# Performance work log

Hardware: AMD Instinct MI355X
Metric: run time of the kernel (lower is better)

Reference implementation:

```python
import jax, jax.numpy as jnp
import numpy as np
from itertools import product

# problem dims
B, D = 2, 80            # batch, grid side -> 2*80^3 = 1.024M voxel slots
N = 200000
CIN, COUT = 32, 64
KV = 27                 # 3x3x3 kernel volume


def _build_rulebook():
    """Submanifold conv rulebook: in_idx[k, j] = input row whose coord equals
    coord_j + offset_k, or N (zero pad row) if that voxel is empty/out of grid."""
    rng = np.random.default_rng(0)
    total = B * D ** 3
    flat = rng.choice(total, size=N, replace=False)
    b, rem = flat // D ** 3, flat % D ** 3
    x, y, z = rem // (D * D), (rem // D) % D, rem % D
    lookup = np.full(total, N, dtype=np.int64)  # empty -> pad index N
    lookup[flat] = np.arange(N)
    rows = []
    for dx, dy, dz in product((-1, 0, 1), repeat=3):  # kernel offsets, dilation=1
        nx, ny, nz = x + dx, y + dy, z + dz
        valid = (0 <= nx) & (nx < D) & (0 <= ny) & (ny < D) & (0 <= nz) & (nz < D)
        nflat = ((b * D + nx) * D + ny) * D + nz
        rows.append(np.where(valid, lookup[np.clip(nflat, 0, total - 1)], N))
    return np.stack(rows).astype(np.int32)  # [KV, N]


def setup_inputs() -> dict:
    key = jax.random.key(0)
    k1, k2, k3 = jax.random.split(key, 3)
    stdv = 1.0 / float(np.sqrt(CIN * KV))  # matches reset_parameters
    feats = jax.random.normal(k1, (N, CIN), dtype=jnp.float32)
    weight = jax.random.uniform(k2, (KV, CIN, COUT), jnp.float32, -stdv, stdv)
    bias = jax.random.uniform(k3, (COUT,), jnp.float32, -stdv, stdv)
    in_idx = jnp.asarray(_build_rulebook())
    return {"feats": feats, "weight": weight, "bias": bias, "in_idx": in_idx}


def reference(feats, weight, bias, in_idx):
    # pad row N = zeros so missing neighbors contribute nothing
    feats_pad = jnp.concatenate(
        [feats, jnp.zeros((1, feats.shape[1]), feats.dtype)], axis=0)  # [N+1, Cin]

    def body(acc, kw):  # scan over the 27 kernel offsets: gather -> matmul -> accumulate
        idx_k, w_k = kw                       # [N] int32, [Cin, Cout]
        return acc + feats_pad[idx_k] @ w_k, None

    out0 = jnp.zeros((feats.shape[0], weight.shape[2]), feats.dtype)  # [N, Cout]
    out, _ = jax.lax.scan(body, out0, (in_idx, weight))
    return out + bias
```

## Files before the change

### kernel.cpp

```cpp
#include <hip/hip_runtime.h>
#include <cstddef>
#include <cstdint>

#define NROWS  200000
#define CIN    32
#define COUT   64
#define KV     27
#define NWAVES (NROWS / 64)

typedef __attribute__((ext_vector_type(8))) short  short8;
typedef __attribute__((ext_vector_type(4))) float  f32x4;

__device__ __forceinline__ unsigned short f2bf(float x) {
  unsigned u = __builtin_bit_cast(unsigned, x);
  u += 0x7FFFu + ((u >> 16) & 1u);
  return (unsigned short)(u >> 16);
}

__global__ void prep_weight_kernel(const float* __restrict__ w,
                                   short8* __restrict__ wsB) {
  int tid = blockIdx.x * blockDim.x + threadIdx.x;
  if (tid >= KV * 4 * 64) return;
  int lane = tid & 63;
  int t    = (tid >> 6) & 3;
  int k    = tid >> 8;
  int col  = t * 16 + (lane & 15);
  int kin0 = (lane >> 4) * 8;
  short8 v;
#pragma unroll
  for (int f = 0; f < 8; ++f)
    v[f] = (short)f2bf(w[((size_t)k * CIN + kin0 + f) * COUT + col]);
  wsB[tid] = v;
}

__global__ void prep_feats_kernel(const float* __restrict__ feats,
                                  short8* __restrict__ fb) {
  int i = blockIdx.x * blockDim.x + threadIdx.x;
  const int total8 = (NROWS + 1) * CIN / 8;
  if (i >= total8) return;
  short8 v = {0, 0, 0, 0, 0, 0, 0, 0};
  if (i < NROWS * CIN / 8) {
    const f32x4* p = (const f32x4*)feats + (size_t)i * 2;
    f32x4 a = p[0], b = p[1];
#pragma unroll
    for (int f = 0; f < 4; ++f) {
      v[f]     = (short)f2bf(a[f]);
      v[4 + f] = (short)f2bf(b[f]);
    }
  }
  fb[i] = v;
}

__global__ __launch_bounds__(256, 3)
void spconv_mfma_kernel(const unsigned short* __restrict__ featsbf,
                        const short8* __restrict__ wsB,
                        const float* __restrict__ bias,
                        const int* __restrict__ in_idx,
                        float* __restrict__ out) {
  __shared__ int sIdx[4][KV][64];

  const int tid  = threadIdx.x;
  const int lane = tid & 63;
  const int w    = tid >> 6;
  const int wid  = (int)blockIdx.x * 4 + w;
  if (wid >= NWAVES) return;
  const int row0 = wid << 6;

  {
    int tmp[KV];
#pragma unroll
    for (int k = 0; k < KV; ++k)
      tmp[k] = in_idx[(size_t)k * NROWS + row0 + lane];
#pragma unroll
    for (int k = 0; k < KV; ++k)
      sIdx[w][k][lane] = tmp[k];
  }

  const int c16  = lane & 15;
  const int kg   = lane >> 4;
  const int koff = kg * 8;

  f32x4 acc[4][4];
#pragma unroll
  for (int t = 0; t < 4; ++t) {
    float bv = bias[t * 16 + c16];
    f32x4 bvv = {bv, bv, bv, bv};
#pragma unroll
    for (int m = 0; m < 4; ++m) acc[m][t] = bvv;
  }

  const short8* bp = wsB + lane;

#pragma unroll 3
  for (int k = 0; k < KV; ++k) {
    int idx[4];
#pragma unroll
    for (int m = 0; m < 4; ++m) idx[m] = sIdx[w][k][m * 16 + c16];

    short8 bfr[4];
#pragma unroll
    for (int t = 0; t < 4; ++t) bfr[t] = bp[(k * 4 + t) * 64];

    short8 afr[4];
#pragma unroll
    for (int m = 0; m < 4; ++m)
      afr[m] = *(const short8*)(featsbf + (size_t)idx[m] * CIN + koff);

#pragma unroll
    for (int m = 0; m < 4; ++m) {
      acc[m][0] = __builtin_amdgcn_mfma_f32_16x16x32_bf16(afr[m], bfr[0], acc[m][0], 0, 0, 0);
      acc[m][1] = __builtin_amdgcn_mfma_f32_16x16x32_bf16(afr[m], bfr[1], acc[m][1], 0, 0, 0);
      acc[m][2] = __builtin_amdgcn_mfma_f32_16x16x32_bf16(afr[m], bfr[2], acc[m][2], 0, 0, 0);
      acc[m][3] = __builtin_amdgcn_mfma_f32_16x16x32_bf16(afr[m], bfr[3], acc[m][3], 0, 0, 0);
    }
  }

#pragma unroll
  for (int m = 0; m < 4; ++m)
#pragma unroll
    for (int t = 0; t < 4; ++t)
#pragma unroll
      for (int r = 0; r < 4; ++r)
        out[(size_t)(row0 + m * 16 + kg * 4 + r) * COUT + t * 16 + c16] = acc[m][t][r];
}

__global__ void spconv_naive_kernel(const float* __restrict__ feats,
                                    const float* __restrict__ w,
                                    const float* __restrict__ bias,
                                    const int* __restrict__ in_idx,
                                    float* __restrict__ out) {
  int gid = blockIdx.x * blockDim.x + threadIdx.x;
  if (gid >= NROWS * COUT) return;
  int row = gid / COUT, co = gid % COUT;
  float acc = bias[co];
  for (int k = 0; k < KV; ++k) {
    int idx = in_idx[(size_t)k * NROWS + row];
    if (idx < NROWS) {
      const float* fr = feats + (size_t)idx * CIN;
      const float* wk = w + (size_t)k * CIN * COUT + co;
#pragma unroll
      for (int c = 0; c < CIN; ++c) acc += fr[c] * wk[(size_t)c * COUT];
    }
  }
  out[gid] = acc;
}

extern "C" void kernel_launch(void* const* d_in, const int* in_sizes, int n_in,
                              void* d_out, int out_size, void* d_ws, size_t ws_size,
                              hipStream_t stream) {
  const float* feats  = (const float*)d_in[0];
  const float* weight = (const float*)d_in[1];
  const float* bias   = (const float*)d_in[2];
  const int*   in_idx = (const int*)d_in[3];
  float*       out    = (float*)d_out;

  const size_t wsB_bytes = (size_t)KV * 4 * 64 * 16;
  const size_t fb_bytes  = (size_t)(NROWS + 1) * CIN * 2;
  short8*         wsB     = (short8*)d_ws;
  unsigned short* featsbf = (unsigned short*)((char*)d_ws + wsB_bytes);

  if (ws_size >= wsB_bytes + fb_bytes) {
    prep_weight_kernel<<<27, 256, 0, stream>>>(weight, wsB);
    prep_feats_kernel<<<((NROWS + 1) * CIN / 8 + 255) / 256, 256, 0, stream>>>(
        feats, (short8*)featsbf);
    const int blocks = (NWAVES + 3) / 4;
    spconv_mfma_kernel<<<blocks, 256, 0, stream>>>(
        featsbf, wsB, bias, in_idx, out);
  } else {
    spconv_naive_kernel<<<(NROWS * COUT + 255) / 256, 256, 0, stream>>>(
        feats, weight, bias, in_idx, out);
  }
}
```

Baseline: 59.07 us.

## Stage all conv weights in LDS and split index staging into halves

Each 768-thread block (12 waves) first copies the full pre-swizzled bf16 weight tensor (27 offsets x 4 column tiles) from global memory into shared memory, so B fragments come from LDS instead of global/L2. To leave LDS room for this, the per-wave rulebook index staging is split into two passes of 14 and 13 offsets that reuse one smaller buffer. The roughly 150 KB of shared memory per block allows only one block per CU, and 261 blocks on 256 CUs leaves a small second round. The launch bound of 3 blocks of 768 threads also squeezes the register budget, which risks spills of the 64-float accumulator.

```diff
diff --git a/kernel.cpp b/kernel.cpp
--- a/kernel.cpp
+++ b/kernel.cpp
@@ -7,6 +7,9 @@
 #define COUT   64
 #define KV     27
 #define NWAVES (NROWS / 64)
+#define WPB    12
+#define TPB    768
+#define KHALF  14
 
 typedef __attribute__((ext_vector_type(8))) short  short8;
 typedef __attribute__((ext_vector_type(4))) float  f32x4;
@@ -51,35 +54,41 @@
   fb[i] = v;
 }
 
-__global__ __launch_bounds__(256, 3)
+__global__ __launch_bounds__(TPB, 3)
 void spconv_mfma_kernel(const unsigned short* __restrict__ featsbf,
                         const short8* __restrict__ wsB,
                         const float* __restrict__ bias,
                         const int* __restrict__ in_idx,
                         float* __restrict__ out) {
-  __shared__ int sIdx[4][KV][64];
-
-  const int tid  = threadIdx.x;
+  __shared__ short8 sB[KV * 4 * 64];
+  __shared__ int sIdx[WPB][KHALF][64];
+
+  const int tid = threadIdx.x;
+#pragma unroll
+  for (int i = 0; i < 9; ++i)
+    sB[i * TPB + tid] = wsB[i * TPB + tid];
+  __syncthreads();
+
   const int lane = tid & 63;
   const int w    = tid >> 6;
-  const int wid  = (int)blockIdx.x * 4 + w;
+  const int wid  = (int)blockIdx.x * WPB + w;
   if (wid >= NWAVES) return;
   const int row0 = wid << 6;
-
-  {
-    int tmp[KV];
-#pragma unroll
-    for (int k = 0; k < KV; ++k)
-      tmp[k] = in_idx[(size_t)k * NROWS + row0 + lane];
-#pragma unroll
-    for (int k = 0; k < KV; ++k)
-      sIdx[w][k][lane] = tmp[k];
-  }
 
   const int c16  = lane & 15;
   const int kg   = lane >> 4;
   const int koff = kg * 8;
 
+  {
+    int tmp[KHALF];
+#pragma unroll
+    for (int k = 0; k < KHALF; ++k)
+      tmp[k] = in_idx[(size_t)k * NROWS + row0 + lane];
+#pragma unroll
+    for (int k = 0; k < KHALF; ++k)
+      sIdx[w][k][lane] = tmp[k];
+  }
+
   f32x4 acc[4][4];
 #pragma unroll
   for (int t = 0; t < 4; ++t) {
@@ -89,17 +98,47 @@
     for (int m = 0; m < 4; ++m) acc[m][t] = bvv;
   }
 
-  const short8* bp = wsB + lane;
-
-#pragma unroll 3
-  for (int k = 0; k < KV; ++k) {
+  for (int k = 0; k < KHALF; ++k) {
     int idx[4];
 #pragma unroll
     for (int m = 0; m < 4; ++m) idx[m] = sIdx[w][k][m * 16 + c16];
 
     short8 bfr[4];
 #pragma unroll
-    for (int t = 0; t < 4; ++t) bfr[t] = bp[(k * 4 + t) * 64];
+    for (int t = 0; t < 4; ++t) bfr[t] = sB[(k * 4 + t) * 64 + lane];
+
+    short8 afr[4];
+#pragma unroll
+    for (int m = 0; m < 4; ++m)
+      afr[m] = *(const short8*)(featsbf + (size_t)idx[m] * CIN + koff);
+
+#pragma unroll
+    for (int m = 0; m < 4; ++m) {
+      acc[m][0] = __builtin_amdgcn_mfma_f32_16x16x32_bf16(afr[m], bfr[0], acc[m][0], 0, 0, 0);
+      acc[m][1] = __builtin_amdgcn_mfma_f32_16x16x32_bf16(afr[m], bfr[1], acc[m][1], 0, 0, 0);
+      acc[m][2] = __builtin_amdgcn_mfma_f32_16x16x32_bf16(afr[m], bfr[2], acc[m][2], 0, 0, 0);
+      acc[m][3] = __builtin_amdgcn_mfma_f32_16x16x32_bf16(afr[m], bfr[3], acc[m][3], 0, 0, 0);
+    }
+  }
+
+  {
+    int tmp[KV - KHALF];
+#pragma unroll
+    for (int j = 0; j < KV - KHALF; ++j)
+      tmp[j] = in_idx[(size_t)(KHALF + j) * NROWS + row0 + lane];
+#pragma unroll
+    for (int j = 0; j < KV - KHALF; ++j)
+      sIdx[w][j][lane] = tmp[j];
+  }
+
+  for (int k = KHALF; k < KV; ++k) {
+    int idx[4];
+#pragma unroll
+    for (int m = 0; m < 4; ++m) idx[m] = sIdx[w][k - KHALF][m * 16 + c16];
+
+    short8 bfr[4];
+#pragma unroll
+    for (int t = 0; t < 4; ++t) bfr[t] = sB[(k * 4 + t) * 64 + lane];
 
     short8 afr[4];
 #pragma unroll
@@ -163,8 +202,8 @@
     prep_weight_kernel<<<27, 256, 0, stream>>>(weight, wsB);
     prep_feats_kernel<<<((NROWS + 1) * CIN / 8 + 255) / 256, 256, 0, stream>>>(
         feats, (short8*)featsbf);
-    const int blocks = (NWAVES + 3) / 4;
-    spconv_mfma_kernel<<<blocks, 256, 0, stream>>>(
+    const int blocks = (NWAVES + WPB - 1) / WPB;
+    spconv_mfma_kernel<<<blocks, TPB, 0, stream>>>(
         featsbf, wsB, bias, in_idx, out);
   } else {
     spconv_naive_kernel<<<(NROWS * COUT + 255) / 256, 256, 0, stream>>>(
```

After: 68.82 us. 16.5% more time.
